# Kernel optimization log

Hardware: AMD Instinct MI355X
Metric: run time of the kernel (lower is better)

The kernel has to match this reference:

```python
import jax, jax.numpy as jnp
import numpy as np

POOLED_H = 7
POOLED_W = 7
SPATIAL_SCALE = 0.5


def _tent_integral(start, end, n):
    """Exact integral of the bilinear basis max(0, 1-|x-i|) over [start, end]
    for every integer grid point i in [0, n). start/end: [...]. Returns [..., n].
    This is the 1D factor of PrRoIPool's closed-form bilinear integral.
    """
    i = jnp.arange(n, dtype=start.dtype)
    a = jnp.clip(start[..., None] - i, -1.0, 1.0)
    b = jnp.clip(end[..., None] - i, -1.0, 1.0)

    def G(t):  # antiderivative of tent, with G(-1) = 0
        return jnp.where(t <= 0.0, 0.5 * (t + 1.0) ** 2, 1.0 - 0.5 * (1.0 - t) ** 2)

    return G(b) - G(a)


def setup_inputs() -> dict:
    key = jax.random.key(0)
    k1, k2, k3, k4 = jax.random.split(key, 4)
    N, C, H, W, R = 8, 256, 56, 56, 256
    features = jax.random.normal(k1, (N, C, H, W), dtype=jnp.float32)
    img_w, img_h = W / SPATIAL_SCALE, H / SPATIAL_SCALE
    bidx = jax.random.randint(k2, (R,), 0, N).astype(jnp.float32)
    xy1 = jax.random.uniform(k3, (R, 2)) * jnp.array([img_w * 0.7, img_h * 0.7], jnp.float32)
    wh = 8.0 + jax.random.uniform(k4, (R, 2)) * jnp.array([img_w * 0.3, img_h * 0.3], jnp.float32)
    rois = jnp.concatenate([bidx[:, None], xy1, xy1 + wh], axis=1)  # (b, x1, y1, x2, y2)
    return {"features": features, "rois": rois}


def reference(features, rois):
    """PrRoIPool2D(7, 7, spatial_scale=0.5): precise (integral) ROI pooling.

    out[r, c, ph, pw] = (1 / bin_area) * \int\int_bin bilinear(F[b_r, c], x, y) dx dy
    which factorizes as Iy^T F Ix with 1D tent-basis integrals.
    """
    N, C, H, W = features.shape
    dt = features.dtype
    batch = rois[:, 0].astype(jnp.int32)
    x1 = rois[:, 1] * SPATIAL_SCALE
    y1 = rois[:, 2] * SPATIAL_SCALE
    x2 = rois[:, 3] * SPATIAL_SCALE
    y2 = rois[:, 4] * SPATIAL_SCALE
    bw = (x2 - x1) / POOLED_W  # [R]
    bh = (y2 - y1) / POOLED_H

    pw = jnp.arange(POOLED_W, dtype=dt)
    ph = jnp.arange(POOLED_H, dtype=dt)
    xs = x1[:, None] + pw * bw[:, None]  # [R, 7] bin left edges
    ys = y1[:, None] + ph * bh[:, None]
    Ix = _tent_integral(xs, xs + bw[:, None], W)  # [R, 7, W]
    Iy = _tent_integral(ys, ys + bh[:, None], H)  # [R, 7, H]

    Fg = features[batch]  # [R, C, H, W] gather of shared map per ROI
    tmp = jnp.einsum('rchw,rqw->rchq', Fg, Ix)   # integrate over x
    acc = jnp.einsum('rph,rchq->rcpq', Iy, tmp)  # integrate over y -> [R, C, 7, 7]

    area = (bw * bh)[:, None, None, None]
    return jnp.where(area > 0.0, acc / jnp.maximum(area, jnp.asarray(1e-12, dt)), 0.0)
```

## Files before the change

### kernel.cpp

```cpp
#include <hip/hip_runtime.h>


#define POOLED 7
#define CPER 32
#define CHUNKS 8
#define NHMAX 24
#define XS 9

__device__ __forceinline__ float Gfun(float t) {
    return (t <= 0.f) ? 0.5f * (t + 1.f) * (t + 1.f)
                      : 1.f - 0.5f * (1.f - t) * (1.f - t);
}
__device__ __forceinline__ float tent_int(float s, float e, float i) {
    float a = fminf(fmaxf(s - i, -1.f), 1.f);
    float b = fminf(fmaxf(e - i, -1.f), 1.f);
    return Gfun(b) - Gfun(a);
}

__global__ __launch_bounds__(256, 8)
void prroi_kernel(const float* __restrict__ F, const float* __restrict__ rois,
                  float* __restrict__ out, int R, int C, int H, int W) {
    const int blk   = blockIdx.x;
    const int r     = blk >> 3;
    const int chunk = blk & (CHUNKS - 1);
    const int wave  = threadIdx.x >> 6;
    const int lane  = threadIdx.x & 63;

    __shared__ float s_wx[4][7][8];
    __shared__ float s_wy[4][7][6];
    __shared__ int   s_ox[4][8];
    __shared__ int   s_oy[4][8];
    __shared__ float s_xint[4][NHMAX][XS];

    const float* roi = rois + (size_t)r * 5;
    const int   b  = (int)roi[0];
    const float x1 = roi[1] * 0.5f, y1 = roi[2] * 0.5f;
    const float x2 = roi[3] * 0.5f, y2 = roi[4] * 0.5f;
    const float bw = (x2 - x1) * (1.f / POOLED);
    const float bh = (y2 - y1) * (1.f / POOLED);
    const float area = bw * bh;
    const float inv_area = (area > 0.f) ? 1.f / fmaxf(area, 1e-12f) : 0.f;

    if (lane < 7) {
        float s = x1 + lane * bw, e = s + bw;
        int o = ((int)ceilf(s - 1.f)) & ~1;
        o = min(max(o, 0), W - 8);
        s_ox[wave][lane] = o;
        #pragma unroll
        for (int k = 0; k < 8; ++k) s_wx[wave][lane][k] = tent_int(s, e, (float)(o + k));
    } else if (lane < 14) {
        int p = lane - 7;
        float s = y1 + p * bh, e = s + bh;
        int o = (int)ceilf(s - 1.f);
        o = min(max(o, 0), H - 6);
        s_oy[wave][p] = o;
        #pragma unroll
        for (int k = 0; k < 6; ++k) s_wy[wave][p][k] = tent_int(s, e, (float)(o + k));
    }
    __syncthreads();

    const int q1 = lane & 7, hs = lane >> 3;
    const bool a1 = (q1 < 7);
    const int qq = a1 ? q1 : 0;
    const int ox1 = s_ox[wave][qq];
    float wx1[8];
    #pragma unroll
    for (int k = 0; k < 8; ++k) wx1[k] = s_wx[wave][qq][k];

    const int p2 = lane >> 3, q2 = lane & 7;
    const bool a2 = (lane < 56) && (q2 < 7);
    const int pp = (p2 < 7) ? p2 : 0;
    const int h0a = s_oy[wave][0];
    const int nh  = s_oy[wave][6] + 6 - h0a;
    const int yo2 = s_oy[wave][pp] - h0a;
    float wy2[6];
    #pragma unroll
    for (int k = 0; k < 6; ++k) wy2[k] = s_wy[wave][pp][k];

    const int c0 = chunk * CPER + wave * (CPER / 4);
    const float* Fb = F + ((size_t)b * C) * H * W;

    for (int i = 0; i < CPER / 4; ++i) {
        const int c = c0 + i;
        const float* Fc = Fb + (size_t)c * H * W;

        #pragma unroll
        for (int it = 0; it < 3; ++it) {
            int hh = it * 8 + hs;
            if (a1 && hh < nh) {
                const float2* rp = (const float2*)(Fc + (h0a + hh) * W + ox1);
                float2 v0 = rp[0], v1 = rp[1], v2 = rp[2], v3 = rp[3];
                float sacc = wx1[0] * v0.x + wx1[1] * v0.y
                           + wx1[2] * v1.x + wx1[3] * v1.y
                           + wx1[4] * v2.x + wx1[5] * v2.y
                           + wx1[6] * v3.x + wx1[7] * v3.y;
                s_xint[wave][hh][q1] = sacc;
            }
        }
        if (a2) {
            float acc = 0.f;
            #pragma unroll
            for (int ky = 0; ky < 6; ++ky)
                acc += wy2[ky] * s_xint[wave][yo2 + ky][q2];
            out[((size_t)r * C + c) * 49 + p2 * 7 + q2] = acc * inv_area;
        }
    }
}

extern "C" void kernel_launch(void* const* d_in, const int* in_sizes, int n_in,
                              void* d_out, int out_size, void* d_ws, size_t ws_size,
                              hipStream_t stream) {
    const float* F    = (const float*)d_in[0];
    const float* rois = (const float*)d_in[1];
    float* out = (float*)d_out;

    const int C = 256, H = 56, W = 56;
    int R = in_sizes[1] / 5;
    dim3 grid(R * CHUNKS), block(256);
    prroi_kernel<<<grid, block, 0, stream>>>(F, rois, out, R, C, H, W);
}
```

Measured before the change: 82.53 us.

## Split channels into 16 chunks, use float4 loads, fold area scale, drop block barrier

The grid doubles to 16 channel chunks per ROI, with 4 channels per wave. This gives more blocks for latency hiding, but each block now does less work while repeating the same setup. The x window offset is aligned to a multiple of 4 so each row is read with two float4 loads instead of four float2 loads. The inverse area is folded into the y weights, which removes a multiply per output. The block-wide barrier is removed and s_xint is double-buffered per wave, which relies on each wave's lanes staying in lockstep when they share their own shared-memory data.

```diff
diff --git a/kernel.cpp b/kernel.cpp
--- a/kernel.cpp
+++ b/kernel.cpp
@@ -2,8 +2,6 @@
 
 
 #define POOLED 7
-#define CPER 32
-#define CHUNKS 8
 #define NHMAX 24
 #define XS 9
 
@@ -19,10 +17,10 @@
 
 __global__ __launch_bounds__(256, 8)
 void prroi_kernel(const float* __restrict__ F, const float* __restrict__ rois,
-                  float* __restrict__ out, int R, int C, int H, int W) {
+                  float* __restrict__ out, int C, int H, int W) {
     const int blk   = blockIdx.x;
-    const int r     = blk >> 3;
-    const int chunk = blk & (CHUNKS - 1);
+    const int r     = blk >> 4;
+    const int chunk = blk & 15;
     const int wave  = threadIdx.x >> 6;
     const int lane  = threadIdx.x & 63;
 
@@ -30,7 +28,7 @@
     __shared__ float s_wy[4][7][6];
     __shared__ int   s_ox[4][8];
     __shared__ int   s_oy[4][8];
-    __shared__ float s_xint[4][NHMAX][XS];
+    __shared__ float s_xint[4][2][NHMAX][XS];
 
     const float* roi = rois + (size_t)r * 5;
     const int   b  = (int)roi[0];
@@ -43,7 +41,7 @@
 
     if (lane < 7) {
         float s = x1 + lane * bw, e = s + bw;
-        int o = ((int)ceilf(s - 1.f)) & ~1;
+        int o = ((int)ceilf(s - 1.f)) & ~3;
         o = min(max(o, 0), W - 8);
         s_ox[wave][lane] = o;
         #pragma unroll
@@ -55,9 +53,8 @@
         o = min(max(o, 0), H - 6);
         s_oy[wave][p] = o;
         #pragma unroll
-        for (int k = 0; k < 6; ++k) s_wy[wave][p][k] = tent_int(s, e, (float)(o + k));
+        for (int k = 0; k < 6; ++k) s_wy[wave][p][k] = tent_int(s, e, (float)(o + k)) * inv_area;
     }
-    __syncthreads();
 
     const int q1 = lane & 7, hs = lane >> 3;
     const bool a1 = (q1 < 7);
@@ -70,39 +67,39 @@
     const int p2 = lane >> 3, q2 = lane & 7;
     const bool a2 = (lane < 56) && (q2 < 7);
     const int pp = (p2 < 7) ? p2 : 0;
-    const int h0a = s_oy[wave][0];
-    const int nh  = s_oy[wave][6] + 6 - h0a;
-    const int yo2 = s_oy[wave][pp] - h0a;
+    const int hb  = s_oy[wave][0];
+    const int nh  = s_oy[wave][6] + 6 - hb;
+    const int yo2 = s_oy[wave][pp] - hb;
     float wy2[6];
     #pragma unroll
     for (int k = 0; k < 6; ++k) wy2[k] = s_wy[wave][pp][k];
 
-    const int c0 = chunk * CPER + wave * (CPER / 4);
+    const int c0 = chunk * 16 + wave * 4;
     const float* Fb = F + ((size_t)b * C) * H * W;
 
-    for (int i = 0; i < CPER / 4; ++i) {
+    #pragma unroll
+    for (int i = 0; i < 4; ++i) {
         const int c = c0 + i;
+        const int buf = i & 1;
         const float* Fc = Fb + (size_t)c * H * W;
 
         #pragma unroll
         for (int it = 0; it < 3; ++it) {
             int hh = it * 8 + hs;
             if (a1 && hh < nh) {
-                const float2* rp = (const float2*)(Fc + (h0a + hh) * W + ox1);
-                float2 v0 = rp[0], v1 = rp[1], v2 = rp[2], v3 = rp[3];
-                float sacc = wx1[0] * v0.x + wx1[1] * v0.y
-                           + wx1[2] * v1.x + wx1[3] * v1.y
-                           + wx1[4] * v2.x + wx1[5] * v2.y
-                           + wx1[6] * v3.x + wx1[7] * v3.y;
-                s_xint[wave][hh][q1] = sacc;
+                const float4* rp = (const float4*)(Fc + (hb + hh) * W + ox1);
+                float4 v0 = rp[0], v1 = rp[1];
+                float s = wx1[0] * v0.x + wx1[1] * v0.y + wx1[2] * v0.z + wx1[3] * v0.w
+                        + wx1[4] * v1.x + wx1[5] * v1.y + wx1[6] * v1.z + wx1[7] * v1.w;
+                s_xint[wave][buf][hh][q1] = s;
             }
         }
         if (a2) {
             float acc = 0.f;
             #pragma unroll
             for (int ky = 0; ky < 6; ++ky)
-                acc += wy2[ky] * s_xint[wave][yo2 + ky][q2];
-            out[((size_t)r * C + c) * 49 + p2 * 7 + q2] = acc * inv_area;
+                acc += wy2[ky] * s_xint[wave][buf][yo2 + ky][q2];
+            out[((size_t)r * C + c) * 49 + p2 * 7 + q2] = acc;
         }
     }
 }
@@ -115,7 +112,6 @@
     float* out = (float*)d_out;
 
     const int C = 256, H = 56, W = 56;
-    int R = in_sizes[1] / 5;
-    dim3 grid(R * CHUNKS), block(256);
-    prroi_kernel<<<grid, block, 0, stream>>>(F, rois, out, R, C, H, W);
+    const int R = in_sizes[1] / 5;
+    prroi_kernel<<<R * 16, 256, 0, stream>>>(F, rois, out, C, H, W);
 }
```

Result: slower. 84.40 us (+2.3%).
